# Performance work log

Measured on AMD Instinct MI355X. Metric: run time of the kernel, lower is better.

The kernel has to match this reference:

```python
import jax, jax.numpy as jnp
import numpy as np

N, E = 4096, 65536
H = 200
KS = (3072, 1536, 768)  # ceil(0.75*4096), ceil(0.5*3072), ceil(0.5*1536)


def _gcn(A, x, W, b):
    # GCNConv with improved=True: A_hat = A + 2I, sym-normalized
    n = A.shape[0]
    Ah = A + 2.0 * jnp.eye(n, dtype=A.dtype)
    dinv = jax.lax.rsqrt(Ah.sum(axis=1))
    An = dinv[:, None] * Ah * dinv[None, :]
    return An @ (x @ W) + b


def _augment(A):
    # GraphUNet.augment_adj: remove self loops, add self loops (w=1), spspmm(A,A), remove self loops
    n = A.shape[0]
    eye = jnp.eye(n, dtype=A.dtype)
    Ap = A * (1.0 - eye) + eye
    A2 = Ap @ Ap  # dense form of spspmm (two-hop adjacency with weights)
    return A2 * (1.0 - eye)


def _pool(A, x, pw, k):
    # TopKPooling: score = tanh(x.w/||w||), keep top-k, scale kept x by score
    score = jnp.tanh((x @ pw) / jnp.linalg.norm(pw))
    val, perm = jax.lax.top_k(score, k)
    return x[perm] * val[:, None], A[perm][:, perm], perm


def _unet(x, adj, w0, b0, w1, b1, w2, b2, w3, b3, p1, p2, p3,
          u0w, u0b, u1w, u1b, u2w, u2b):
    down = [(w1, b1), (w2, b2), (w3, b3)]
    pws = [p1, p2, p3]
    up = [(u0w, u0b), (u1w, u1b), (u2w, u2b)]
    x = jax.nn.relu(_gcn(adj, x, w0, b0))
    xs, As, perms = [x], [adj], []
    A = adj
    for i in range(3):
        A = _augment(A)
        x, A, perm = _pool(A, x, pws[i], KS[i])
        x = jax.nn.relu(_gcn(A, x, *down[i]))
        if i < 2:
            xs.append(x)
            As.append(A)
        perms.append(perm)
    for i in range(3):
        j = 2 - i
        upf = jnp.zeros_like(xs[j]).at[perms[j]].set(x)
        x = xs[j] + upf  # sum_res=True
        x = _gcn(As[j], x, *up[i])
        if i < 2:
            x = jax.nn.relu(x)
    return jax.nn.log_softmax(x, axis=1)


def setup_inputs() -> dict:
    key = jax.random.key(0)
    ks = jax.random.split(key, 16)
    x = jax.random.normal(ks[0], (N, 3), dtype=jnp.float32)
    src = jax.random.randint(ks[1], (E,), 0, N)
    dst = jax.random.randint(ks[2], (E,), 0, N)
    A = jnp.zeros((N, N), jnp.float32).at[src, dst].set(1.0)
    A = jnp.maximum(A, A.T) * (1.0 - jnp.eye(N, dtype=jnp.float32))
    g = lambda k, s: jax.random.normal(k, s, jnp.float32) * 0.1
    z = lambda n: jnp.zeros((n,), jnp.float32)
    return dict(
        x=x, adj=A,
        w0=g(ks[3], (3, H)), b0=z(H),
        w1=g(ks[4], (H, H)), b1=z(H),
        w2=g(ks[5], (H, H)), b2=z(H),
        w3=g(ks[6], (H, H)), b3=z(H),
        p1=g(ks[7], (H,)), p2=g(ks[8], (H,)), p3=g(ks[9], (H,)),
        u0w=g(ks[10], (H, H)), u0b=z(H),
        u1w=g(ks[11], (H, H)), u1b=z(H),
        u2w=g(ks[12], (H, 2)), u2b=z(2),
    )


def reference(x, adj, w0, b0, w1, b1, w2, b2, w3, b3, p1, p2, p3,
              u0w, u0b, u1w, u1b, u2w, u2b):
    return _unet(x, adj, w0, b0, w1, b1, w2, b2, w3, b3, p1, p2, p3,
                 u0w, u0b, u1w, u1b, u2w, u2b)
```

## Files before the change

### kernel.cpp

```cpp
#include <hip/hip_runtime.h>

typedef unsigned short u16;
typedef unsigned int u32;
typedef unsigned long long u64;
typedef signed char s8;
typedef __attribute__((ext_vector_type(8))) short bfrag8;
typedef __attribute__((ext_vector_type(4))) float f32x4;
typedef __attribute__((ext_vector_type(4))) int i32x4;
typedef __attribute__((address_space(1))) const void gconst_void;
typedef __attribute__((address_space(3))) void lds_void_t;

__device__ __forceinline__ float bf2f(u16 u) {
  return __uint_as_float(((u32)u) << 16);
}
__device__ __forceinline__ u16 f2bf(float f) {
  u32 u = __float_as_uint(f);
  u32 r = (u + 0x7FFFu + ((u >> 16) & 1u)) >> 16;
  return (u16)r;
}
__device__ __forceinline__ void split3(float v, u16& hi, u16& mi, u16& lo) {
  hi = f2bf(v); float r1 = v - bf2f(hi);
  mi = f2bf(r1); float r2 = r1 - bf2f(mi);
  lo = f2bf(r2);
}
__device__ __forceinline__ float ld1(const void* p, int isbf, long idx) {
  return isbf ? bf2f(((const u16*)p)[idx]) : ((const float*)p)[idx];
}
__device__ __forceinline__ void ld4(const void* p, int isbf, long base, long gc, long bound, float v[4]) {
  if (gc + 3 < bound && ((base & 3) == 0)) {
    if (isbf) {
      const ushort4 u = *(const ushort4*)((const u16*)p + base);
      v[0] = bf2f(u.x); v[1] = bf2f(u.y); v[2] = bf2f(u.z); v[3] = bf2f(u.w);
    } else {
      const float4 f = *(const float4*)((const float*)p + base);
      v[0] = f.x; v[1] = f.y; v[2] = f.z; v[3] = f.w;
    }
  } else {
    #pragma unroll
    for (int d = 0; d < 4; ++d) v[d] = (gc + d < bound) ? ld1(p, isbf, base + d) : 0.f;
  }
}

__global__ void detect_k(const u32* __restrict__ a, long nw, int* __restrict__ flag) {
  long nv = nw >> 2;
  long stride = (long)gridDim.x * 256;
  int f = 0;
  for (long j = (long)blockIdx.x * 256 + threadIdx.x; j < nv; j += stride) {
    uint4 w = ((const uint4*)a)[j];
    if (w.x == 0x00003F80u || w.x == 0x3F803F80u ||
        w.y == 0x00003F80u || w.y == 0x3F803F80u ||
        w.z == 0x00003F80u || w.z == 0x3F803F80u ||
        w.w == 0x00003F80u || w.w == 0x3F803F80u) f = 1;
  }
  if (__any(f)) {
    if ((threadIdx.x & 63) == 0) atomicOr(flag, 1);
  }
}

__device__ __forceinline__ int get_bf(int abf, const int* dtf) {
  return (abf >= 0) ? abf : *dtf;
}

__device__ __forceinline__ void stageB16(const void* g, void* lds) {
#if __has_builtin(__builtin_amdgcn_global_load_lds)
  __builtin_amdgcn_global_load_lds((gconst_void*)g, (lds_void_t*)lds, 16, 0, 0);
#else
  int lane = threadIdx.x & 63;
  *(int4*)((char*)lds + lane * 16) = *(const int4*)g;
#endif
}

template<typename PT>
__global__ __launch_bounds__(256) void syrk_tri_i8_parts(
    const s8* __restrict__ Ag, int ldk, int Ksplit, int ntri,
    PT* __restrict__ parts)
{
  __shared__ s8 At[2][128 * 64];
  __shared__ s8 Bt[2][128 * 64];
  const int t = blockIdx.x;
  int ti = (int)((sqrtf((float)(8 * t + 1)) - 1.0f) * 0.5f);
  while ((ti + 1) * (ti + 2) / 2 <= t) ++ti;
  while (ti * (ti + 1) / 2 > t) --ti;
  const int tj = t - ti * (ti + 1) / 2;

  const int tid = threadIdx.x;
  const int wave = tid >> 6, lane = tid & 63;
  const int wr = wave >> 1, wc = wave & 1;
  const long rowA0 = (long)ti * 128;
  const long rowB0 = (long)tj * 128;
  const int kbeg = blockIdx.y * Ksplit;
  const int nsteps = Ksplit / 64;

  i32x4 acc[4][4];
  #pragma unroll
  for (int i = 0; i < 4; ++i)
    #pragma unroll
    for (int j = 0; j < 4; ++j) acc[i][j] = (i32x4)0;

  const int srow = lane >> 2;
  const int scol = (lane & 3) * 16;
  const int m = lane & 15, q = lane >> 4;

  auto stage = [&](int buf, int k0) {
    #pragma unroll
    for (int tt = 0; tt < 2; ++tt) {
      const int r = wave * 32 + tt * 16;
      stageB16(Ag + (rowA0 + r + srow) * (long)ldk + k0 + scol, At[buf] + r * 64);
      stageB16(Ag + (rowB0 + r + srow) * (long)ldk + k0 + scol, Bt[buf] + r * 64);
    }
  };

  stage(0, kbeg);
  __syncthreads();
  int cur = 0;
  for (int st = 0; st < nsteps; ++st) {
    if (st + 1 < nsteps) stage(cur ^ 1, kbeg + (st + 1) * 64);

    i32x4 af[4], bf[4];
    #pragma unroll
    for (int mt = 0; mt < 4; ++mt)
      af[mt] = *(const i32x4*)(At[cur] + (wr * 64 + mt * 16 + m) * 64 + q * 16);
    #pragma unroll
    for (int nt = 0; nt < 4; ++nt)
      bf[nt] = *(const i32x4*)(Bt[cur] + (wc * 64 + nt * 16 + m) * 64 + q * 16);
    #pragma unroll
    for (int mt = 0; mt < 4; ++mt)
      #pragma unroll
      for (int nt = 0; nt < 4; ++nt)
        acc[mt][nt] = __builtin_amdgcn_mfma_i32_16x16x64_i8(af[mt], bf[nt], acc[mt][nt], 0, 0, 0);
    if (st + 1 < nsteps) __syncthreads();
    cur ^= 1;
  }

  PT* P = parts + ((long)blockIdx.y * ntri + t) * 16384;
  #pragma unroll
  for (int mt = 0; mt < 4; ++mt) {
    #pragma unroll
    for (int nt = 0; nt < 4; ++nt) {
      const int r0 = wr * 64 + mt * 16 + q * 4;
      const int c = wc * 64 + nt * 16 + m;
      #pragma unroll
      for (int r = 0; r < 4; ++r)
        P[(r0 + r) * 128 + c] = (PT)acc[mt][nt][r];
    }
  }
}

template<typename PT>
__global__ __launch_bounds__(256) void reduce_tri_i8_k(
    const PT* __restrict__ parts, int ntri, int n, int nz,
    u16* __restrict__ Ah, u16* __restrict__ Al, double* __restrict__ rs)
{
  __shared__ float T[128 * 33];
  const int t = blockIdx.x >> 2;
  const int slab = blockIdx.x & 3;
  int ti = (int)((sqrtf((float)(8 * t + 1)) - 1.0f) * 0.5f);
  while ((ti + 1) * (ti + 2) / 2 <= t) ++ti;
  while (ti * (ti + 1) / 2 > t) --ti;
  const int tj = t - ti * (ti + 1) / 2;
  const long rowA0 = (long)ti * 128;
  const long rowB0 = (long)tj * 128;
  const int r0 = slab * 32;
  const int tid = threadIdx.x;
  const int lane = tid & 63;
  const long tstride = (long)ntri * 16384;

  #pragma unroll
  for (int it = 0; it < 16; ++it) {
    const int idx = it * 256 + tid;
    const int lr = idx >> 7;
    const int lc = idx & 127;
    long base = (long)t * 16384 + (r0 + lr) * 128 + lc;
    int v = 0;
    for (int z = 0; z < nz; ++z) v += (int)parts[(long)z * tstride + base];
    const long gr = rowA0 + r0 + lr;
    const long gc = rowB0 + lc;
    if (gr == gc) v = 0;
    const float fv = (float)v;
    const u16 h = f2bf(fv);
    const long o = gr * n + gc;
    Ah[o] = h;
    if (Al) Al[o] = f2bf(fv - bf2f(h));
    T[lc * 33 + lr] = fv;
    float wsum = fv;
    #pragma unroll
    for (int off = 32; off > 0; off >>= 1) wsum += __shfl_down(wsum, off);
    if (lane == 0) atomicAdd(&rs[gr], (double)wsum);
  }
  if (ti == tj) return;
  __syncthreads();
  #pragma unroll
  for (int it = 0; it < 16; ++it) {
    const int idx = it * 256 + tid;
    const int mr = idx >> 5;
    const int mc = idx & 31;
    const float fv = T[mr * 33 + mc];
    const u16 h = f2bf(fv);
    const long o = (rowB0 + mr) * n + rowA0 + r0 + mc;
    Ah[o] = h;
    if (Al) Al[o] = f2bf(fv - bf2f(h));
    float ws = fv;
    #pragma unroll
    for (int off = 16; off > 0; off >>= 1) ws += __shfl_down(ws, off);
    if ((lane & 31) == 0) atomicAdd(&rs[rowB0 + mr], (double)ws);
  }
}

__global__ __launch_bounds__(256) void syrk_tri2_parts(
    const u16* __restrict__ Ah, const u16* __restrict__ Al, int ldk,
    float* __restrict__ parts, int n, int per)
{
  __shared__ u16 Ath[2][128 * 32];
  __shared__ u16 Bth[2][128 * 32];
  __shared__ u16 Atl[2][128 * 32];
  __shared__ u16 Btl[2][128 * 32];
  const int t = blockIdx.x;
  int ti = (int)((sqrtf((float)(8 * t + 1)) - 1.0f) * 0.5f);
  while ((ti + 1) * (ti + 2) / 2 <= t) ++ti;
  while (ti * (ti + 1) / 2 > t) --ti;
  const int tj = t - ti * (ti + 1) / 2;

  const int tid = threadIdx.x;
  const int wave = tid >> 6, lane = tid & 63;
  const int wr = wave >> 1, wc = wave & 1;
  const long rowA0 = (long)ti * 128;
  const long rowB0 = (long)tj * 128;
  const int kbeg = blockIdx.y * per;
  const int nsteps = per / 32;

  f32x4 acc[4][4];
  #pragma unroll
  for (int i = 0; i < 4; ++i)
    #pragma unroll
    for (int j = 0; j < 4; ++j) acc[i][j] = (f32x4)0.f;

  const int srow = lane >> 2;
  const int scol = (lane & 3) * 8;
  const int m = lane & 15, q = lane >> 4;

  auto stage = [&](int buf, int k0) {
    #pragma unroll
    for (int tt = 0; tt < 2; ++tt) {
      const int r = wave * 32 + tt * 16;
      stageB16(Ah + (rowA0 + r + srow) * (long)ldk + k0 + scol, Ath[buf] + r * 32);
      stageB16(Ah + (rowB0 + r + srow) * (long)ldk + k0 + scol, Bth[buf] + r * 32);
      stageB16(Al + (rowA0 + r + srow) * (long)ldk + k0 + scol, Atl[buf] + r * 32);
      stageB16(Al + (rowB0 + r + srow) * (long)ldk + k0 + scol, Btl[buf] + r * 32);
    }
  };

  stage(0, kbeg);
  __syncthreads();
  int cur = 0;
  for (int st = 0; st < nsteps; ++st) {
    if (st + 1 < nsteps) stage(cur ^ 1, kbeg + (st + 1) * 32);

    bfrag8 afh[4], afl[4], bfh[4], bfl[4];
    #pragma unroll
    for (int mt = 0; mt < 4; ++mt) {
      afh[mt] = *(const bfrag8*)(Ath[cur] + (wr * 64 + mt * 16 + m) * 32 + q * 8);
      afl[mt] = *(const bfrag8*)(Atl[cur] + (wr * 64 + mt * 16 + m) * 32 + q * 8);
    }
    #pragma unroll
    for (int nt = 0; nt < 4; ++nt) {
      bfh[nt] = *(const bfrag8*)(Bth[cur] + (wc * 64 + nt * 16 + m) * 32 + q * 8);
      bfl[nt] = *(const bfrag8*)(Btl[cur] + (wc * 64 + nt * 16 + m) * 32 + q * 8);
    }
    #pragma unroll
    for (int mt = 0; mt < 4; ++mt)
      #pragma unroll
      for (int nt = 0; nt < 4; ++nt) {
        acc[mt][nt] = __builtin_amdgcn_mfma_f32_16x16x32_bf16(afh[mt], bfh[nt], acc[mt][nt], 0, 0, 0);
        acc[mt][nt] = __builtin_amdgcn_mfma_f32_16x16x32_bf16(afh[mt], bfl[nt], acc[mt][nt], 0, 0, 0);
        acc[mt][nt] = __builtin_amdgcn_mfma_f32_16x16x32_bf16(afl[mt], bfh[nt], acc[mt][nt], 0, 0, 0);
        acc[mt][nt] = __builtin_amdgcn_mfma_f32_16x16x32_bf16(afl[mt], bfl[nt], acc[mt][nt], 0, 0, 0);
      }
    if (st + 1 < nsteps) __syncthreads();
    cur ^= 1;
  }

  float* P = parts + (long)blockIdx.y * n * n;
  #pragma unroll
  for (int mt = 0; mt < 4; ++mt) {
    #pragma unroll
    for (int nt = 0; nt < 4; ++nt) {
      const long gr0 = rowA0 + wr * 64 + mt * 16 + q * 4;
      const long gc = rowB0 + wc * 64 + nt * 16 + m;
      #pragma unroll
      for (int r = 0; r < 4; ++r)
        P[(gr0 + r) * n + gc] = acc[mt][nt][r];
    }
  }
}

__global__ void reduce_tri_mirror_k(const float* __restrict__ parts,
                                    u16* __restrict__ Ah, u16* __restrict__ Al,
                                    double* __restrict__ rsum, int n, int nz) {
  __shared__ double red[256];
  const int tid = threadIdx.x;
  long idx = (long)blockIdx.x * 256 + tid;
  long nn = (long)n * n;
  long r = idx / n, c = idx - r * n;
  double myv = 0.0;
  if (idx < nn) {
    if (r == c) {
      Ah[idx] = 0; Al[idx] = 0;
    } else if (r > c) {
      float s = 0.f;
      for (int z = 0; z < nz; ++z) s += parts[(long)z * nn + r * n + c];
      long mi = c * n + r;
      u16 h = f2bf(s);
      u16 l = f2bf(s - bf2f(h));
      Ah[idx] = h; Al[idx] = l;
      Ah[mi] = h;  Al[mi] = l;
      myv = (double)s;
      atomicAdd(&rsum[c], (double)s);
    }
  }
  red[tid] = myv;
  __syncthreads();
  for (int st = 128; st > 0; st >>= 1) {
    if (tid < st) red[tid] += red[tid + st];
    __syncthreads();
  }
  if (tid == 0 && idx < nn) atomicAdd(&rsum[r], red[0]);
}

__global__ void bg_i8_k(const void* __restrict__ src, int srcbf, int nsrc,
                        const int* __restrict__ perm, int kRows,
                        s8* __restrict__ Ag, const int* __restrict__ dtf,
                        const float* __restrict__ xsrc, const float* __restrict__ score,
                        float* __restrict__ xdst, unsigned nbB) {
  if (blockIdx.x < nbB) {
    long tot4 = ((long)kRows * nsrc) >> 2;
    long i4 = (long)blockIdx.x * 256 + threadIdx.x;
    if (i4 >= tot4) return;
    long idx = i4 << 2;
    int r = (int)(idx / nsrc);
    int c = (int)(idx - (long)r * nsrc);
    int p = perm[r];
    float v[4];
    if (get_bf(srcbf, dtf)) {
      ushort4 u = *(const ushort4*)((const u16*)src + (long)p * nsrc + c);
      v[0] = bf2f(u.x); v[1] = bf2f(u.y); v[2] = bf2f(u.z); v[3] = bf2f(u.w);
    } else {
      float4 f = *(const float4*)((const float*)src + (long)p * nsrc + c);
      v[0] = f.x; v[1] = f.y; v[2] = f.z; v[3] = f.w;
    }
    char4 o;
    o.x = (s8)(int)(v[0] + ((c + 0 == p) ? 1.f : 0.f));
    o.y = (s8)(int)(v[1] + ((c + 1 == p) ? 1.f : 0.f));
    o.z = (s8)(int)(v[2] + ((c + 2 == p) ? 1.f : 0.f));
    o.w = (s8)(int)(v[3] + ((c + 3 == p) ? 1.f : 0.f));
    *(char4*)(Ag + idx) = o;
  } else {
    long tot4 = (long)kRows * 50;
    long i4 = (long)(blockIdx.x - nbB) * 256 + threadIdx.x;
    if (i4 >= tot4) return;
    long idx = i4 << 2;
    int r = (int)(idx / 200);
    int c = (int)(idx - (long)r * 200);
    int p = perm[r];
    float4 x = *(const float4*)(xsrc + (long)p * 200 + c);
    float sc = score[p];
    x.x *= sc; x.y *= sc; x.z *= sc; x.w *= sc;
    *(float4*)(xdst + idx) = x;
  }
}

__global__ void bg_sp_k(const u16* __restrict__ srcH, const u16* __restrict__ srcL,
                        int nsrc, const int* __restrict__ perm, int kRows,
                        u16* __restrict__ Agh, u16* __restrict__ Agl,
                        const float* __restrict__ xsrc, const float* __restrict__ score,
                        float* __restrict__ xdst, unsigned nbB) {
  if (blockIdx.x < nbB) {
    long tot4 = ((long)kRows * nsrc) >> 2;
    long i4 = (long)blockIdx.x * 256 + threadIdx.x;
    if (i4 >= tot4) return;
    long idx = i4 << 2;
    int r = (int)(idx / nsrc);
    int c = (int)(idx - (long)r * nsrc);
    int p = perm[r];
    long si = (long)p * nsrc + c;
    ushort4 uh = *(const ushort4*)(srcH + si);
    ushort4 ul = *(const ushort4*)(srcL + si);
    ushort4 oh, ol;
    {
      float v = bf2f(uh.x) + bf2f(ul.x); if (c + 0 == p) v += 1.f;
      oh.x = f2bf(v); ol.x = f2bf(v - bf2f(oh.x));
    }
    {
      float v = bf2f(uh.y) + bf2f(ul.y); if (c + 1 == p) v += 1.f;
      oh.y = f2bf(v); ol.y = f2bf(v - bf2f(oh.y));
    }
    {
      float v = bf2f(uh.z) + bf2f(ul.z); if (c + 2 == p) v += 1.f;
      oh.z = f2bf(v); ol.z = f2bf(v - bf2f(oh.z));
    }
    {
      float v = bf2f(uh.w) + bf2f(ul.w); if (c + 3 == p) v += 1.f;
      oh.w = f2bf(v); ol.w = f2bf(v - bf2f(oh.w));
    }
    *(ushort4*)(Agh + idx) = oh;
    *(ushort4*)(Agl + idx) = ol;
  } else {
    long tot4 = (long)kRows * 50;
    long i4 = (long)(blockIdx.x - nbB) * 256 + threadIdx.x;
    if (i4 >= tot4) return;
    long idx = i4 << 2;
    int r = (int)(idx / 200);
    int c = (int)(idx - (long)r * 200);
    int p = perm[r];
    float4 x = *(const float4*)(xsrc + (long)p * 200 + c);
    float sc = score[p];
    x.x *= sc; x.y *= sc; x.z *= sc; x.w *= sc;
    *(float4*)(xdst + idx) = x;
  }
}

template<int HASAL>
__global__ __launch_bounds__(512, 4) void agg_mfma8z(
    const u16* __restrict__ Ah, const u16* __restrict__ Al,
    const u16* __restrict__ ZT, float* __restrict__ parts,
    int K, int per_steps)
{
  __shared__ u16 At[2][8 * 512];
  __shared__ u16 Alt[HASAL ? 2 * 8 * 512 : 2];
  __shared__ u16 Zt[2][21 * 512];

  const int tid = threadIdx.x;
  const int wave = tid >> 6, lane = tid & 63;
  const int zh = blockIdx.z;
  const int ct0 = zh ? 7 : 0;
  const int nts = zh ? 6 : 7;
  const int cth = (nts + 1) >> 1;
  const int rg = wave & 3;
  const int cg = wave >> 2;
  const int wct0 = cg ? cth : 0;
  const int wnct = cg ? (nts - cth) : cth;
  const long row0 = (long)blockIdx.x * 128;
  const int chunk = blockIdx.y;
  const int kbeg = chunk * per_steps * 32;
  const int nsteps = (min(K, kbeg + per_steps * 32) - kbeg) / 32;
  const int m = lane & 15, q = lane >> 4;
  const int srow = lane >> 2, scol = (lane & 3) * 8;
  const int nstg = (HASAL ? 16 : 8) + 3 * nts;

  auto stage = [&](int buf, int k0) {
    for (int s = wave; s < nstg; s += 8) {
      if (s < 8) {
        stageB16(Ah + (row0 + s * 16 + srow) * (long)K + k0 + scol, At[buf] + s * 512);
      } else if (HASAL && s < 16) {
        stageB16(Al + (row0 + (s - 8) * 16 + srow) * (long)K + k0 + scol,
                 (u16*)Alt + (buf * 8 + (s - 8)) * 512);
      } else {
        const int zz = s - (HASAL ? 16 : 8);
        const int pl = (zz >= 2 * nts) ? 2 : ((zz >= nts) ? 1 : 0);
        const int c = zz - pl * nts;
        stageB16(ZT + ((long)(pl * 208 + (ct0 + c) * 16 + srow)) * K + k0 + scol,
                 Zt[buf] + (pl * 7 + c) * 512);
      }
    }
  };

  f32x4 acc[2][4];
  #pragma unroll
  for (int rt = 0; rt < 2; ++rt)
    #pragma unroll
    for (int ct = 0; ct < 4; ++ct) acc[rt][ct] = (f32x4)0.f;

  stage(0, kbeg);
  __syncthreads();
  int cur = 0;
  for (int t = 0; t < nsteps; ++t) {
    if (t + 1 < nsteps) stage(cur ^ 1, kbeg + (t + 1) * 32);

    const u16* Atb = At[cur];
    const u16* Ztb = Zt[cur];
    bfrag8 af0 = *(const bfrag8*)(Atb + (rg * 2) * 512 + m * 32 + q * 8);
    bfrag8 af1 = *(const bfrag8*)(Atb + (rg * 2 + 1) * 512 + m * 32 + q * 8);
    bfrag8 al0, al1;
    if (HASAL) {
      const u16* Altb = (const u16*)Alt + cur * 8 * 512;
      al0 = *(const bfrag8*)(Altb + (rg * 2) * 512 + m * 32 + q * 8);
      al1 = *(const bfrag8*)(Altb + (rg * 2 + 1) * 512 + m * 32 + q * 8);
    }
    #pragma unroll
    for (int ct = 0; ct < 4; ++ct) {
      if (ct < wnct) {
        const int gct = wct0 + ct;
        bfrag8 b0 = *(const bfrag8*)(Ztb + (0 * 7 + gct) * 512 + m * 32 + q * 8);
        bfrag8 b1 = *(const bfrag8*)(Ztb + (1 * 7 + gct) * 512 + m * 32 + q * 8);
        bfrag8 b2 = *(const bfrag8*)(Ztb + (2 * 7 + gct) * 512 + m * 32 + q * 8);
        acc[0][ct] = __builtin_amdgcn_mfma_f32_16x16x32_bf16(af0, b0, acc[0][ct], 0, 0, 0);
        acc[0][ct] = __builtin_amdgcn_mfma_f32_16x16x32_bf16(af0, b1, acc[0][ct], 0, 0, 0);
        acc[0][ct] = __builtin_amdgcn_mfma_f32_16x16x32_bf16(af0, b2, acc[0][ct], 0, 0, 0);
        acc[1][ct] = __builtin_amdgcn_mfma_f32_16x16x32_bf16(af1, b0, acc[1][ct], 0, 0, 0);
        acc[1][ct] = __builtin_amdgcn_mfma_f32_16x16x32_bf16(af1, b1, acc[1][ct], 0, 0, 0);
        acc[1][ct] = __builtin_amdgcn_mfma_f32_16x16x32_bf16(af1, b2, acc[1][ct], 0, 0, 0);
        if (HASAL) {
          acc[0][ct] = __builtin_amdgcn_mfma_f32_16x16x32_bf16(al0, b0, acc[0][ct], 0, 0, 0);
          acc[0][ct] = __builtin_amdgcn_mfma_f32_16x16x32_bf16(al0, b1, acc[0][ct], 0, 0, 0);
          acc[1][ct] = __builtin_amdgcn_mfma_f32_16x16x32_bf16(al1, b0, acc[1][ct], 0, 0, 0);
          acc[1][ct] = __builtin_amdgcn_mfma_f32_16x16x32_bf16(al1, b1, acc[1][ct], 0, 0, 0);
        }
      }
    }
    if (t + 1 < nsteps) __syncthreads();
    cur ^= 1;
  }

  float* P = parts + (long)chunk * gridDim.x * 128 * 208;
  #pragma unroll
  for (int rt = 0; rt < 2; ++rt) {
    #pragma unroll
    for (int ct = 0; ct < 4; ++ct) {
      if (ct < wnct) {
        const long grow0 = row0 + rg * 32 + rt * 16 + q * 4;
        const long gcol = (ct0 + wct0 + ct) * 16 + m;
        #pragma unroll
        for (int r = 0; r < 4; ++r)
          P[(grow0 + r) * 208 + gcol] = acc[rt][ct][r];
      }
    }
  }
}

__global__ __launch_bounds__(256) void reduce_epi_k(
    const float* __restrict__ parts, const float* __restrict__ Zs,
    const double* __restrict__ rs, const float* __restrict__ b,
    float* __restrict__ out, int n, int nz, int relu,
    const float* __restrict__ pw, float* __restrict__ score)
{
  __shared__ float vrow[200];
  const int i = blockIdx.x, tid = threadIdx.x;
  float dv = (float)(1.0 / sqrt(rs[i] + 2.0));
  if (tid < 200) {
    long base = (long)i * 208 + tid;
    float s = 0.f;
    for (int c = 0; c < nz; ++c) s += parts[(long)c * n * 208 + base];
    float v = dv * (s + 2.f * Zs[(long)i * 200 + tid]) + b[tid];
    if (relu) v = fmaxf(v, 0.f);
    out[(long)i * 200 + tid] = v;
    if (score) vrow[tid] = v;
  }
  if (!score) return;
  __syncthreads();
  if (tid < 64) {
    double ps = 0.0;
    for (int j = tid; j < 200; j += 64) { double w = pw[j]; ps += w * w; }
    for (int off = 32; off > 0; off >>= 1) ps += __shfl_down(ps, off);
    double nrm = sqrt(__shfl(ps, 0));
    double s = 0.0;
    for (int j = tid; j < 200; j += 64) s += (double)vrow[j] * (double)pw[j];
    for (int off = 32; off > 0; off >>= 1) s += __shfl_down(s, off);
    if (tid == 0) score[i] = (float)tanh(s / nrm);
  }
}

__global__ void a_from_adj_rs_k(const void* __restrict__ adj, const int* __restrict__ dtf,
                                int n, u16* __restrict__ Ah, double* __restrict__ rs) {
  __shared__ double red[256];
  int bf = *dtf;
  const int row = blockIdx.x, tid = threadIdx.x;
  const long base = (long)row * n;
  double s = 0.0;
  if (bf) {
    const uint4* src = (const uint4*)((const u16*)adj + base);
    uint4* dst = (uint4*)(Ah + base);
    for (int j = tid; j < (n >> 3); j += 256) {
      uint4 v = src[j];
      dst[j] = v;
      s += (double)(bf2f((u16)(v.x & 0xFFFFu)) + bf2f((u16)(v.x >> 16))
                  + bf2f((u16)(v.y & 0xFFFFu)) + bf2f((u16)(v.y >> 16))
                  + bf2f((u16)(v.z & 0xFFFFu)) + bf2f((u16)(v.z >> 16))
                  + bf2f((u16)(v.w & 0xFFFFu)) + bf2f((u16)(v.w >> 16)));
    }
  } else {
    const float4* src = (const float4*)((const float*)adj + base);
    ushort4* dst = (ushort4*)(Ah + base);
    for (int j = tid; j < (n >> 2); j += 256) {
      float4 v = src[j];
      ushort4 o;
      o.x = f2bf(v.x); o.y = f2bf(v.y); o.z = f2bf(v.z); o.w = f2bf(v.w);
      dst[j] = o;
      s += (double)(v.x + v.y + v.z + v.w);
    }
  }
  red[tid] = s; __syncthreads();
  for (int st = 128; st > 0; st >>= 1) {
    if (tid < st) red[tid] += red[tid + st];
    __syncthreads();
  }
  if (tid == 0) rs[row] = red[0];
}

__global__ __launch_bounds__(256) void gemm64_f64(
    const void* __restrict__ Ap, long lda, int abf,
    const void* __restrict__ Bp, long ldb, int bbf,
    float* __restrict__ C, long ldc, int M, int N, int K,
    const double* __restrict__ rsum, u16* __restrict__ ZT, const int* __restrict__ dtf,
    const float* __restrict__ ua_pool, const int* __restrict__ ua_inv)
{
  const int abf_ = get_bf(abf, dtf);
  const int bbf_ = get_bf(bbf, dtf);
  __shared__ float As[16][64];
  __shared__ float Bs[16][64];
  const int tid = threadIdx.x;
  const int tr = tid >> 4, tc = tid & 15;
  const long row0 = (long)blockIdx.y * 64;
  const long col0 = (long)blockIdx.x * 64;
  double acc[4][4];
  #pragma unroll
  for (int i = 0; i < 4; ++i)
    #pragma unroll
    for (int j = 0; j < 4; ++j) acc[i][j] = 0.0;

  const int am = tid >> 2;
  const int ak = (tid & 3) * 4;
  const int bk = tid >> 4;
  const int bn = (tid & 15) * 4;
  const long gmA = row0 + am;
  const int uar = (ua_inv && gmA < M) ? ua_inv[gmA] : -1;

  for (int k0 = 0; k0 < K; k0 += 16) {
    float va[4] = {0.f, 0.f, 0.f, 0.f};
    {
      long gm = row0 + am; long gk = k0 + ak;
      if (gm < M && gk < K) {
        if (ua_inv) {
          float4 x = *(const float4*)((const float*)Ap + gm * lda + gk);
          if (uar >= 0) {
            const float4 pv = *(const float4*)(ua_pool + (long)uar * lda + gk);
            x.x += pv.x; x.y += pv.y; x.z += pv.z; x.w += pv.w;
          }
          va[0] = x.x; va[1] = x.y; va[2] = x.z; va[3] = x.w;
        } else {
          ld4(Ap, abf_, gm * lda + gk, gk, K, va);
        }
      }
    }
    As[ak + 0][am] = va[0]; As[ak + 1][am] = va[1];
    As[ak + 2][am] = va[2]; As[ak + 3][am] = va[3];

    float vb[4] = {0.f, 0.f, 0.f, 0.f};
    {
      long gk = k0 + bk; long gn = col0 + bn;
      if (gk < K && gn < N) ld4(Bp, bbf_, gk * ldb + gn, gn, N, vb);
    }
    Bs[bk][bn + 0] = vb[0]; Bs[bk][bn + 1] = vb[1];
    Bs[bk][bn + 2] = vb[2]; Bs[bk][bn + 3] = vb[3];

    __syncthreads();
    #pragma unroll
    for (int kk = 0; kk < 16; ++kk) {
      float a[4], b[4];
      #pragma unroll
      for (int i = 0; i < 4; ++i) a[i] = As[kk][tr * 4 + i];
      #pragma unroll
      for (int j = 0; j < 4; ++j) b[j] = Bs[kk][tc * 4 + j];
      #pragma unroll
      for (int i = 0; i < 4; ++i)
        #pragma unroll
        for (int j = 0; j < 4; ++j)
          acc[i][j] += (double)a[i] * (double)b[j];
    }
    __syncthreads();
  }
  #pragma unroll
  for (int i = 0; i < 4; ++i) {
    long gm = row0 + tr * 4 + i;
    if (gm >= M) continue;
    float sc = rsum ? (float)(1.0 / sqrt(rsum[gm] + 2.0)) : 1.f;
    #pragma unroll
    for (int j = 0; j < 4; ++j) {
      long gn = col0 + tc * 4 + j;
      if (gn < N) {
        float v0 = (float)acc[i][j];
        float v = v0 * sc;
        C[gm * ldc + gn] = v;
        if (ZT) {
          u16 hi, mi, lo; split3(v, hi, mi, lo);
          ZT[((long)0 * 208 + gn) * M + gm] = hi;
          ZT[((long)1 * 208 + gn) * M + gm] = mi;
          ZT[((long)2 * 208 + gn) * M + gm] = lo;
        }
      }
    }
  }
}

struct UpBatch {
  const void* src[19];
  float* dst[19];
  int n[19];
};

__global__ void upcast_batch_k(UpBatch ub, const int* __restrict__ dtf) {
  int bf = *dtf;
  int a = blockIdx.y;
  int i = blockIdx.x * 256 + threadIdx.x;
  if (i < ub.n[a]) ub.dst[a][i] = ld1(ub.src[a], bf, i);
}

__global__ __launch_bounds__(256) void rank_part_k(
    const float* __restrict__ score, int n, int ns, int* __restrict__ prank)
{
  __shared__ u64 sk[256];
  const int tid = threadIdx.x;
  const int s = blockIdx.x;
  const int slice = n / ns;
  const int jb = s * slice;
  for (int j = tid; j < slice; j += 256) {
    int gj = jb + j;
    u32 b = __float_as_uint(score[gj]);
    u32 u = (b & 0x80000000u) ? ~b : (b | 0x80000000u);
    sk[j] = ((u64)u << 32) | (u32)(~(u32)gj);
  }
  __syncthreads();
  const int i0 = tid * 16;
  if (i0 >= n) return;
  u64 myk[16];
  int cnt[16];
  #pragma unroll
  for (int e = 0; e < 16; ++e) {
    int i = i0 + e;
    u64 key = 0ULL;
    if (i < n) {
      u32 b = __float_as_uint(score[i]);
      u32 u = (b & 0x80000000u) ? ~b : (b | 0x80000000u);
      key = ((u64)u << 32) | (u32)(~(u32)i);
    }
    myk[e] = key; cnt[e] = 0;
  }
  #pragma unroll 4
  for (int j = 0; j < slice; ++j) {
    u64 kj = sk[j];
    #pragma unroll
    for (int e = 0; e < 16; ++e) cnt[e] += (kj > myk[e]) ? 1 : 0;
  }
  #pragma unroll
  for (int e = 0; e < 16; ++e) {
    int i = i0 + e;
    if (i < n) prank[s * n + i] = cnt[e];
  }
}

__global__ void rank_scatter_k(const int* __restrict__ prank, int n, int ns, int k,
                               int* __restrict__ perm, int* __restrict__ inv) {
  int i = blockIdx.x * 256 + threadIdx.x;
  if (i >= n) return;
  int r = 0;
  for (int s = 0; s < ns; ++s) r += prank[s * n + i];
  inv[i] = (r < k) ? r : -1;
  if (r < k) perm[r] = i;
}

__global__ void matvec2_final_k(const void* __restrict__ A, int abf, int n,
                                const float* __restrict__ Zs, const double* __restrict__ rs0,
                                const float* __restrict__ b2, float* __restrict__ out,
                                const int* __restrict__ dtf) {
  const int bf = get_bf(abf, dtf);
  int row = blockIdx.x, tid = threadIdx.x;
  const long base = (long)row * n;
  double s0 = 0.0, s1 = 0.0;
  for (int j4 = tid; j4 < (n >> 2); j4 += 256) {
    const int j = j4 << 2;
    float a0, a1, a2, a3;
    if (bf) {
      ushort4 u = *(const ushort4*)((const u16*)A + base + j);
      a0 = bf2f(u.x); a1 = bf2f(u.y); a2 = bf2f(u.z); a3 = bf2f(u.w);
    } else {
      float4 f = *(const float4*)((const float*)A + base + j);
      a0 = f.x; a1 = f.y; a2 = f.z; a3 = f.w;
    }
    const float4 z01 = *(const float4*)(Zs + 2 * j);
    const float4 z23 = *(const float4*)(Zs + 2 * j + 4);
    s0 += (double)a0 * (double)z01.x; s1 += (double)a0 * (double)z01.y;
    s0 += (double)a1 * (double)z01.z; s1 += (double)a1 * (double)z01.w;
    s0 += (double)a2 * (double)z23.x; s1 += (double)a2 * (double)z23.y;
    s0 += (double)a3 * (double)z23.z; s1 += (double)a3 * (double)z23.w;
  }
  __shared__ double r0[256], r1[256];
  r0[tid] = s0; r1[tid] = s1; __syncthreads();
  for (int st = 128; st > 0; st >>= 1) {
    if (tid < st) { r0[tid] += r0[tid + st]; r1[tid] += r1[tid + st]; }
    __syncthreads();
  }
  if (tid == 0) {
    double y0 = (double)((float)r0[0]);
    double y1 = (double)((float)r1[0]);
    double di = (double)((float)(1.0 / sqrt(rs0[row] + 2.0)));
    double t0 = di * (y0 + 2.0 * (double)Zs[2 * row]) + (double)b2[0];
    double t1 = di * (y1 + 2.0 * (double)Zs[2 * row + 1]) + (double)b2[1];
    double mx = fmax(t0, t1);
    double l = mx + log(exp(t0 - mx) + exp(t1 - mx));
    out[2 * row] = (float)(t0 - l);
    out[2 * row + 1] = (float)(t1 - l);
  }
}

extern "C" void kernel_launch(void* const* d_in, const int* in_sizes, int n_in,
                              void* d_out, int out_size, void* d_ws, size_t ws_size,
                              hipStream_t stream) {
  const int N0 = 4096, H = 200;
  const int K1 = 3072, K2 = 1536, K3 = 768;
  const int TK_NS = 64;

  const void* in_x = d_in[0];
  const void* adj  = d_in[1];
  const void* w0 = d_in[2];  const void* b0 = d_in[3];
  const void* w1 = d_in[4];  const void* b1 = d_in[5];
  const void* w2 = d_in[6];  const void* b2 = d_in[7];
  const void* w3 = d_in[8];  const void* b3 = d_in[9];
  const void* p1 = d_in[10]; const void* p2 = d_in[11];
  const void* p3 = d_in[12];
  const void* u0w = d_in[13]; const void* u0b = d_in[14];
  const void* u1w = d_in[15]; const void* u1b = d_in[16];
  const void* u2w = d_in[17]; const void* u2b = d_in[18];

  char* wp = (char*)d_ws;
  auto alloc = [&](size_t bytes) -> void* {
    void* p = (void*)wp;
    wp += (bytes + 255) & ~(size_t)255;
    return p;
  };
  size_t partsBytes = (size_t)300 * 4 * 16384 * 4 + 1024;
  float* parts = (float*)alloc(partsBytes);
  s8*    Agb  = (s8*)alloc((size_t)K1 * N0);
  u16* Ag3h = (u16*)alloc((size_t)K3 * K2 * 2);
  u16* Ag3l = (u16*)alloc((size_t)K3 * K2 * 2);
  u16* Ah0 = (u16*)alloc((size_t)N0 * N0 * 2);
  u16* Ah1 = (u16*)alloc((size_t)K1 * K1 * 2);
  u16* Ah2 = (u16*)alloc((size_t)K2 * K2 * 2);
  u16* Al2 = (u16*)alloc((size_t)K2 * K2 * 2);
  u16* Ah3 = (u16*)alloc((size_t)K3 * K3 * 2);
  u16* Al3 = (u16*)alloc((size_t)K3 * K3 * 2);
  u16* ZT  = (u16*)alloc((size_t)3 * 208 * N0 * 2);
  float* xs0  = (float*)alloc((size_t)N0 * H * 4);
  float* xs1  = (float*)alloc((size_t)K1 * H * 4);
  float* xs2  = (float*)alloc((size_t)K2 * H * 4);
  float* xcur = (float*)alloc((size_t)N0 * H * 4);
  float* xtmp = (float*)alloc((size_t)N0 * H * 4);
  float* Zbuf = (float*)alloc((size_t)N0 * H * 4);
  float* Xinf = (float*)alloc((size_t)N0 * 3 * 4);
  double* rs0 = (double*)alloc((size_t)N0 * 8);
  double* rs1 = (double*)alloc((size_t)K1 * 8);
  double* rs2 = (double*)alloc((size_t)K2 * 8);
  double* rs3 = (double*)alloc((size_t)K3 * 8);
  int* dtflag = (int*)alloc(256);
  float* scores = (float*)alloc((size_t)N0 * 4);
  int* prank = (int*)alloc((size_t)TK_NS * N0 * 4);
  int* perm1 = (int*)alloc((size_t)K1 * 4);
  int* perm2 = (int*)alloc((size_t)K2 * 4);
  int* perm3 = (int*)alloc((size_t)K3 * 4);
  int* inv1 = (int*)alloc((size_t)N0 * 4);
  int* inv2 = (int*)alloc((size_t)K1 * 4);
  int* inv3 = (int*)alloc((size_t)K2 * 4);
  float* w0f = (float*)alloc(3 * H * 4);  float* b0f = (float*)alloc(H * 4);
  float* w1f = (float*)alloc(H * H * 4);  float* b1f = (float*)alloc(H * 4);
  float* w2f = (float*)alloc(H * H * 4);  float* b2f = (float*)alloc(H * 4);
  float* w3f = (float*)alloc(H * H * 4);  float* b3f = (float*)alloc(H * 4);
  float* p1f = (float*)alloc(H * 4);
  float* p2f = (float*)alloc(H * 4);
  float* p3f = (float*)alloc(H * 4);
  float* u0wf = (float*)alloc(H * H * 4); float* u0bf = (float*)alloc(H * 4);
  float* u1wf = (float*)alloc(H * H * 4); float* u1bf = (float*)alloc(H * 4);
  float* u2wf = (float*)alloc(H * 2 * 4); float* u2bf = (float*)alloc(2 * 4);
  (void)in_sizes; (void)n_in; (void)out_size; (void)ws_size; (void)xtmp;

  hipMemsetAsync(rs1, 0, (size_t)(K1 + K2 + K3) * 8 + 256, stream);
  detect_k<<<dim3(2048), dim3(256), 0, stream>>>((const u32*)adj, (long)N0 * N0 / 2, dtflag);

  {
    UpBatch ub;
    const void* srcs[19] = {in_x, w0, b0, w1, b1, w2, b2, w3, b3, p1, p2, p3,
                            u0w, u0b, u1w, u1b, u2w, u2b, u2b};
    float* dsts[19] = {Xinf, w0f, b0f, w1f, b1f, w2f, b2f, w3f, b3f, p1f, p2f, p3f,
                       u0wf, u0bf, u1wf, u1bf, u2wf, u2bf, u2bf};
    int ns[19] = {N0 * 3, 3 * H, H, H * H, H, H * H, H, H * H, H, H, H, H,
                  H * H, H, H * H, H, H * 2, 2, 2};
    for (int i = 0; i < 19; ++i) { ub.src[i] = srcs[i]; ub.dst[i] = dsts[i]; ub.n[i] = ns[i]; }
    upcast_batch_k<<<dim3((N0 * 3 + 255) / 256, 19), dim3(256), 0, stream>>>(ub, dtflag);
  }

  a_from_adj_rs_k<<<dim3(N0), dim3(256), 0, stream>>>(adj, dtflag, N0, Ah0, rs0);

  auto gemm64 = [&](const void* A, long lda, int abf, const void* B, long ldb, int bbf,
                    float* C, long ldc, int M, int Nn, int K, const double* rsum, u16* zt,
                    const float* uaPool, const int* uaInv) {
    dim3 g((Nn + 63) / 64, (M + 63) / 64);
    gemm64_f64<<<g, dim3(256), 0, stream>>>(A, lda, abf, B, ldb, bbf, C, ldc, M, Nn, K,
                                            rsum, zt, dtflag, uaPool, uaInv);
  };

  auto gcn = [&](const u16* Ah, const u16* Al, int n, int chunks, const double* rs,
                 const float* Xin_, int din, const float* W, const float* bb,
                 float* out, const float* pwf, float* scoreOut,
                 const float* uaPool, const int* uaInv) {
    gemm64(Xin_, din, 0, W, H, 0, Zbuf, H, n, H, din, rs, ZT, uaPool, uaInv);
    if (Al)
      agg_mfma8z<1><<<dim3(n / 128, chunks, 2), dim3(512), 0, stream>>>(
          Ah, Al, ZT, parts, n, (n / 32) / chunks);
    else
      agg_mfma8z<0><<<dim3(n / 128, chunks, 2), dim3(512), 0, stream>>>(
          Ah, nullptr, ZT, parts, n, (n / 32) / chunks);
    reduce_epi_k<<<dim3(n), dim3(256), 0, stream>>>(
        parts, Zbuf, rs, bb, out, n, chunks, 1, pwf, scoreOut);
  };

  auto topk = [&](const float* sc, int n, int k, int* perm, int* inv) {
    rank_part_k<<<dim3(TK_NS), dim3(256), 0, stream>>>(sc, n, TK_NS, prank);
    rank_scatter_k<<<dim3((unsigned)((n + 255) / 256)), dim3(256), 0, stream>>>(
        prank, n, TK_NS, k, perm, inv);
  };

  gcn(Ah0, nullptr, N0, 8, rs0, Xinf, 3, w0f, b0f, xs0, p1f, scores, nullptr, nullptr);

  topk(scores, N0, K1, perm1, inv1);
  {
    unsigned nbB = (unsigned)(((long)K1 * N0 / 4 + 255) / 256);
    unsigned nbG = (unsigned)(((long)K1 * 50 + 255) / 256);
    bg_i8_k<<<dim3(nbB + nbG), dim3(256), 0, stream>>>(
        Ah0, 1, N0, perm1, K1, Agb, dtflag, xs0, scores, xcur, nbB);
    int nt = K1 / 128;
    int ntri = nt * (nt + 1) / 2;
    syrk_tri_i8_parts<short><<<dim3(ntri, 4), dim3(256), 0, stream>>>(
        Agb, N0, N0 / 4, ntri, (short*)parts);
    reduce_tri_i8_k<short><<<dim3(ntri * 4), dim3(256), 0, stream>>>(
        (const short*)parts, ntri, K1, 4, Ah1, nullptr, rs1);
  }
  gcn(Ah1, nullptr, K1, 8, rs1, xcur, H, w1f, b1f, xs1, p2f, scores, nullptr, nullptr);

  topk(scores, K1, K2, perm2, inv2);
  {
    unsigned nbB = (unsigned)(((long)K2 * K1 / 4 + 255) / 256);
    unsigned nbG = (unsigned)(((long)K2 * 50 + 255) / 256);
    bg_i8_k<<<dim3(nbB + nbG), dim3(256), 0, stream>>>(
        Ah1, 1, K1, perm2, K2, Agb, dtflag, xs1, scores, xcur, nbB);
    int nt = K2 / 128;
    int ntri = nt * (nt + 1) / 2;
    syrk_tri_i8_parts<int><<<dim3(ntri, 8), dim3(256), 0, stream>>>(
        Agb, K1, K1 / 8, ntri, (int*)parts);
    reduce_tri_i8_k<int><<<dim3(ntri * 4), dim3(256), 0, stream>>>(
        (const int*)parts, ntri, K2, 8, Ah2, Al2, rs2);
  }
  gcn(Ah2, Al2, K2, 12, rs2, xcur, H, w2f, b2f, xs2, p3f, scores, nullptr, nullptr);

  topk(scores, K2, K3, perm3, inv3);
  {
    unsigned nbB = (unsigned)(((long)K3 * K2 / 4 + 255) / 256);
    unsigned nbG = (unsigned)(((long)K3 * 50 + 255) / 256);
    bg_sp_k<<<dim3(nbB + nbG), dim3(256), 0, stream>>>(
        Ah2, Al2, K2, perm3, K3, Ag3h, Ag3l, xs2, scores, xcur, nbB);
    int nt = K3 / 128;
    syrk_tri2_parts<<<dim3(nt * (nt + 1) / 2, 8), dim3(256), 0, stream>>>(
        Ag3h, Ag3l, K2, parts, K3, K2 / 8);
    long nn = (long)K3 * K3;
    reduce_tri_mirror_k<<<dim3((unsigned)(nn / 256)), dim3(256), 0, stream>>>(
        parts, Ah3, Al3, rs3, K3, 8);
  }
  gcn(Ah3, Al3, K3, 24, rs3, xcur, H, w3f, b3f, xcur, nullptr, nullptr, nullptr, nullptr);

  gcn(Ah2, Al2, K2, 12, rs2, xs2, H, u0wf, u0bf, xcur, nullptr, nullptr, xcur, inv3);

  gcn(Ah1, nullptr, K1, 8, rs1, xs1, H, u1wf, u1bf, xcur, nullptr, nullptr, xcur, inv2);

  gemm64(xs0, H, 0, u2wf, 2, 0, Zbuf, 2, N0, 2, H, rs0, nullptr, xcur, inv1);
  matvec2_final_k<<<dim3(N0), dim3(256), 0, stream>>>(
      Ah0, 1, N0, Zbuf, rs0, u2bf, (float*)d_out, dtflag);
}
```

Measured before the change: 769.4 us.

## Fuse split-K SYRK and reduction into single full-K triangular kernel for level one

Replaces the split-K int8 SYRK that wrote partial tiles, plus the separate reduction kernel, with one kernel per triangular tile. Each tile runs the whole K loop and writes the bf16 adjacency for both the tile and its mirror (transposed through LDS). Row sums are accumulated with double atomics. This removes the round trip of partial sums through memory and one launch, but cuts the grid to a quarter of the blocks. Each block now does a long serial K loop, and the atomics assume rs1 is zeroed beforehand.

```diff
diff --git a/kernel.cpp b/kernel.cpp
--- a/kernel.cpp
+++ b/kernel.cpp
@@ -68,6 +68,122 @@
   int lane = threadIdx.x & 63;
   *(int4*)((char*)lds + lane * 16) = *(const int4*)g;
 #endif
+}
+
+__global__ __launch_bounds__(256) void syrk_tri_i8_full(
+    const s8* __restrict__ Ag, int ldk, int K, int ldc,
+    u16* __restrict__ Ah, u16* __restrict__ Al, double* __restrict__ rsum)
+{
+  __shared__ s8 At[2][128 * 64];
+  __shared__ s8 Bt[2][128 * 64];
+  __shared__ int tb[4][16][17];
+  const int t = blockIdx.x;
+  int ti = (int)((sqrtf((float)(8 * t + 1)) - 1.0f) * 0.5f);
+  while ((ti + 1) * (ti + 2) / 2 <= t) ++ti;
+  while (ti * (ti + 1) / 2 > t) --ti;
+  const int tj = t - ti * (ti + 1) / 2;
+
+  const int tid = threadIdx.x;
+  const int wave = tid >> 6, lane = tid & 63;
+  const int wr = wave >> 1, wc = wave & 1;
+  const long rowA0 = (long)ti * 128;
+  const long rowB0 = (long)tj * 128;
+  const int nsteps = K / 64;
+
+  i32x4 acc[4][4];
+  #pragma unroll
+  for (int i = 0; i < 4; ++i)
+    #pragma unroll
+    for (int j = 0; j < 4; ++j) acc[i][j] = (i32x4)0;
+
+  const int srow = lane >> 2;
+  const int scol = (lane & 3) * 16;
+  const int m = lane & 15, q = lane >> 4;
+
+  auto stage = [&](int buf, int k0) {
+    #pragma unroll
+    for (int tt = 0; tt < 2; ++tt) {
+      const int r = wave * 32 + tt * 16;
+      stageB16(Ag + (rowA0 + r + srow) * (long)ldk + k0 + scol, At[buf] + r * 64);
+      stageB16(Ag + (rowB0 + r + srow) * (long)ldk + k0 + scol, Bt[buf] + r * 64);
+    }
+  };
+
+  stage(0, 0);
+  __syncthreads();
+  int cur = 0;
+  for (int st = 0; st < nsteps; ++st) {
+    if (st + 1 < nsteps) stage(cur ^ 1, (st + 1) * 64);
+
+    i32x4 af[4], bf[4];
+    #pragma unroll
+    for (int mt = 0; mt < 4; ++mt)
+      af[mt] = *(const i32x4*)(At[cur] + (wr * 64 + mt * 16 + m) * 64 + q * 16);
+    #pragma unroll
+    for (int nt = 0; nt < 4; ++nt)
+      bf[nt] = *(const i32x4*)(Bt[cur] + (wc * 64 + nt * 16 + m) * 64 + q * 16);
+    #pragma unroll
+    for (int mt = 0; mt < 4; ++mt)
+      #pragma unroll
+      for (int nt = 0; nt < 4; ++nt)
+        acc[mt][nt] = __builtin_amdgcn_mfma_i32_16x16x64_i8(af[mt], bf[nt], acc[mt][nt], 0, 0, 0);
+    if (st + 1 < nsteps) __syncthreads();
+    cur ^= 1;
+  }
+
+  #pragma unroll
+  for (int mt = 0; mt < 4; ++mt) {
+    double rp[4] = {0.0, 0.0, 0.0, 0.0};
+    #pragma unroll
+    for (int nt = 0; nt < 4; ++nt) {
+      const long gr0 = rowA0 + wr * 64 + mt * 16 + q * 4;
+      const long gc = rowB0 + wc * 64 + nt * 16 + m;
+      #pragma unroll
+      for (int r = 0; r < 4; ++r) {
+        const long gr = gr0 + r;
+        int iv = (gr == gc) ? 0 : acc[mt][nt][r];
+        float fv = (float)iv;
+        long idx = gr * ldc + gc;
+        u16 h = f2bf(fv);
+        Ah[idx] = h;
+        if (Al) Al[idx] = f2bf(fv - bf2f(h));
+        rp[r] += (double)iv;
+      }
+    }
+    #pragma unroll
+    for (int r = 0; r < 4; ++r) {
+      double v = rp[r];
+      for (int off = 8; off > 0; off >>= 1) v += __shfl_down(v, off);
+      if (m == 0) atomicAdd(&rsum[rowA0 + wr * 64 + mt * 16 + q * 4 + r], v);
+    }
+  }
+  if (ti != tj) {
+    #pragma unroll
+    for (int nt = 0; nt < 4; ++nt) {
+      double cp = 0.0;
+      #pragma unroll
+      for (int mt = 0; mt < 4; ++mt) {
+        #pragma unroll
+        for (int r = 0; r < 4; ++r) tb[wave][q * 4 + r][m] = acc[mt][nt][r];
+        const long baseR = rowB0 + wc * 64 + nt * 16;
+        const long baseC = rowA0 + wr * 64 + mt * 16;
+        #pragma unroll
+        for (int r = 0; r < 4; ++r) {
+          float tv = (float)tb[wave][m][q * 4 + r];
+          long idx = (baseR + q * 4 + r) * ldc + baseC + m;
+          u16 h = f2bf(tv);
+          Ah[idx] = h;
+          if (Al) Al[idx] = f2bf(tv - bf2f(h));
+        }
+        #pragma unroll
+        for (int r = 0; r < 4; ++r) cp += (double)acc[mt][nt][r];
+      }
+      double v = cp;
+      v += __shfl_down(v, 32);
+      v += __shfl_down(v, 16);
+      if (q == 0) atomicAdd(&rsum[rowB0 + wc * 64 + nt * 16 + m], v);
+    }
+  }
 }
 
 template<typename PT>
@@ -925,10 +1041,8 @@
         Ah0, 1, N0, perm1, K1, Agb, dtflag, xs0, scores, xcur, nbB);
     int nt = K1 / 128;
     int ntri = nt * (nt + 1) / 2;
-    syrk_tri_i8_parts<short><<<dim3(ntri, 4), dim3(256), 0, stream>>>(
-        Agb, N0, N0 / 4, ntri, (short*)parts);
-    reduce_tri_i8_k<short><<<dim3(ntri * 4), dim3(256), 0, stream>>>(
-        (const short*)parts, ntri, K1, 4, Ah1, nullptr, rs1);
+    syrk_tri_i8_full<<<dim3(ntri), dim3(256), 0, stream>>>(
+        Agb, N0, N0, K1, Ah1, nullptr, rs1);
   }
   gcn(Ah1, nullptr, K1, 8, rs1, xcur, H, w1f, b1f, xs1, p2f, scores, nullptr, nullptr);
 
```

New measurement: 753.3 us. 1.02x faster.
